# Kernel optimization log

Hardware: AMD Instinct MI355X
Metric: run time of the kernel (lower is better)

## Reference

```python
import jax, jax.numpy as jnp
import numpy as np

B, K, N, D = 64, 64, 32768, 2048   # batch, knn neighbors, memory size, feat dim (hardcoded 2048 in source)
NC, NHID, TOPK = 2048, 512, 5      # num clusters, gcn hidden, topk in affinity masking


def setup_inputs() -> dict:
    key = jax.random.key(0)
    ks = jax.random.split(key, 8)
    features = jax.random.normal(ks[0], (N, D), jnp.float32)
    labels = jax.random.randint(ks[1], (N,), 0, NC)
    indexes = jax.random.randint(ks[2], (B,), 0, N)
    ori_knn_neighbor = jax.random.randint(ks[3], (B, K), 0, N)
    s = 0.02
    conv_w = jax.random.normal(ks[4], (2 * D, NHID), jnp.float32) * s
    conv_b = jnp.zeros((NHID,), jnp.float32)
    w1 = jax.random.normal(ks[5], (NHID, NHID), jnp.float32) * s
    b1 = jnp.zeros((NHID,), jnp.float32)
    prelu_a = jnp.full((NHID,), 0.25, jnp.float32)
    w2 = jax.random.normal(ks[6], (NHID, 2), jnp.float32) * s
    b2 = jnp.zeros((2,), jnp.float32)
    return dict(indexes=indexes, features=features, labels=labels,
                ori_knn_neighbor=ori_knn_neighbor, conv_w=conv_w, conv_b=conv_b,
                w1=w1, b1=b1, prelu_a=prelu_a, w2=w2, b2=b2)


def _build_graphs(indexes, features, labels, ori_knn_neighbor):
    # cluster mean features (index_add_ + count normalize), done under no_grad in torch
    counts = jax.ops.segment_sum(jnp.ones((N,), jnp.float32), labels, num_segments=NC)
    clu_sum = jax.ops.segment_sum(features, labels, num_segments=NC)
    clu_mean = clu_sum / jnp.maximum(counts, 1.0)[:, None]

    def per_sample(idx, nbr):
        clu_lab = labels[nbr]                                  # [K]
        cf = clu_mean[clu_lab].at[0].set(features[idx])        # [K, D]
        A = (cf @ cf.T) / 5.0                                  # [K, K]
        j = jnp.arange(K)
        # keep only first occurrence of each cluster label (np.unique return_index)
        dup = jnp.any((clu_lab[:, None] == clu_lab[None, :]) & (j[None, :] < j[:, None]), axis=1)
        keep = (~dup).astype(A.dtype)                          # [K]
        _, ti = jax.lax.top_k(A, TOPK)                         # [K, TOPK]
        m = jnp.zeros_like(A).at[j[:, None], ti].set(1.0)
        m = ((m > 0) & (m.T > 0)).astype(A.dtype) * keep[:, None] * keep[None, :]
        A = A * m
        cf = cf / jnp.linalg.norm(cf, axis=1, keepdims=True)   # row-normalize
        cf = cf - cf[0]                                        # center on query (row 0 -> 0)
        return cf, A

    x, adj = jax.vmap(per_sample)(indexes, ori_knn_neighbor)   # [B,K,D], [B,K,K]
    return jax.lax.stop_gradient(x), jax.lax.stop_gradient(adj)


def reference(indexes, features, labels, ori_knn_neighbor,
              conv_w, conv_b, w1, b1, prelu_a, w2, b2):
    x, adj = _build_graphs(indexes, features, labels, ori_knn_neighbor)
    # GraphConv with MeanAggregator: agg = A @ x, concat, linear, relu
    agg = jnp.einsum('bij,bjd->bid', adj, x)                   # [B,K,D]
    h = jax.nn.relu(jnp.concatenate([x, agg], axis=-1) @ conv_w + conv_b)  # [B,K,NHID]
    h0 = h.reshape(-1, NHID)
    h1 = h0 @ w1 + b1
    h1 = jnp.where(h1 > 0, h1, prelu_a * h1)                   # PReLU(nhid)
    logits = h1 @ w2 + b2                                      # [B*K, 2]
    return jax.nn.softmax(logits.reshape(B, K, 2), axis=2)
```

## Files before the change

### kernel.cpp

```cpp
#include <hip/hip_runtime.h>
#include <hip/hip_bf16.h>

#define BB 64
#define KN 64
#define NPTS 32768
#define DD 2048
#define NCC 2048
#define NH 512
#define MM 4096
#define K2 4096

typedef unsigned short u16;
typedef unsigned int u32;
typedef __attribute__((ext_vector_type(8))) short short8;
typedef __attribute__((ext_vector_type(4))) float f32x4;

__device__ __forceinline__ float bf2f(u32 u){
  union { u32 i; float f; } v; v.i = u << 16; return v.f;
}
__device__ __forceinline__ u16 f2bf(float f){
  union { float f; u32 i; } v; v.f = f;
  u32 x = v.i;
  return (u16)((x + 0x7fffu + ((x >> 16) & 1u)) >> 16);
}

typedef __attribute__((address_space(3))) u32 as3_u32;
typedef const __attribute__((address_space(1))) u32 as1_u32;
__device__ __forceinline__ void glds16(const void* g, void* l){
  __builtin_amdgcn_global_load_lds((as1_u32*)g, (as3_u32*)l, 16, 0, 0);
}

__global__ __launch_bounds__(256) void k_prep(
    const int* __restrict__ labels, int* __restrict__ counts,
    const int* __restrict__ knn, int* __restrict__ used,
    const void* __restrict__ conv_w, u16* __restrict__ cwT, int fcw,
    const void* __restrict__ w1, u16* __restrict__ w1T, int fw1){
  __shared__ u16 tile[64][65];
  int bb = blockIdx.x, t = threadIdx.x;
  if(bb < 128){
    int n = bb*256 + t;
    atomicAdd(&counts[labels[n]], 1);
    return;
  }
  if(bb == 704){
    #pragma unroll
    for(int i=0;i<16;i++){
      int idx = i*256 + t;
      used[labels[knn[idx]]] = 1;
    }
    return;
  }
  const void* src; u16* dst; int Kd, Nd, isf32, tb;
  if(bb < 640){ src=conv_w; dst=cwT; Kd=K2; Nd=NH; isf32=fcw; tb=bb-128; }
  else        { src=w1;     dst=w1T; Kd=NH; Nd=NH; isf32=fw1; tb=bb-640; }
  int nbt = Nd >> 6;
  int k0 = (tb / nbt) << 6;
  int n0 = (tb % nbt) << 6;
  if(isf32){
    const float* s = (const float*)src;
    #pragma unroll
    for(int ph=0; ph<16; ph++){
      int idx = ph*256 + t;
      int r = idx >> 6, c = idx & 63;
      tile[r][c] = f2bf(s[(size_t)(k0+r)*Nd + n0 + c]);
    }
  } else {
    const u16* s = (const u16*)src;
    #pragma unroll
    for(int ph=0; ph<16; ph++){
      int idx = ph*256 + t;
      int r = idx >> 6, c = idx & 63;
      tile[r][c] = s[(size_t)(k0+r)*Nd + n0 + c];
    }
  }
  __syncthreads();
  #pragma unroll
  for(int ph=0; ph<16; ph++){
    int idx = ph*256 + t;
    int r = idx >> 6, c = idx & 63;
    dst[(size_t)(n0+r)*Kd + k0 + c] = tile[c][r];
  }
}

__global__ void k_scan(const int* __restrict__ counts, int* __restrict__ offsets){
  __shared__ int sb[256];
  int t = threadIdx.x;
  int c[8]; int s = 0;
  #pragma unroll
  for(int i=0;i<8;i++){ c[i] = counts[t*8+i]; s += c[i]; }
  sb[t] = s; __syncthreads();
  int v = s;
  for(int off=1; off<256; off<<=1){
    int u = (t>=off) ? sb[t-off] : 0;
    __syncthreads();
    v += u; sb[t] = v;
    __syncthreads();
  }
  int run = v - s;
  #pragma unroll
  for(int i=0;i<8;i++){ offsets[t*8+i] = run; run += c[i]; }
}

__global__ void k_scatter(const int* __restrict__ labels, const int* __restrict__ offsets,
                          int* __restrict__ cursor, int* __restrict__ sorted){
  int n = blockIdx.x*256 + threadIdx.x;
  int c = labels[n];
  int p = atomicAdd(&cursor[c], 1);
  sorted[offsets[c] + p] = n;
}

__global__ __launch_bounds__(256) void k_clumean(
    const void* __restrict__ feat, const int* __restrict__ counts,
    const int* __restrict__ offsets, const int* __restrict__ sorted,
    const int* __restrict__ used, int isf32, float* __restrict__ clu){
  int c = blockIdx.x, t = threadIdx.x;
  if(!used[c]) return;
  __shared__ int ridx[64];
  int cnt = counts[c], start = offsets[c];
  float acc[8] = {0,0,0,0,0,0,0,0};
  for(int base=0; base<cnt; base+=64){
    int take = min(64, cnt-base);
    __syncthreads();
    if(t < take) ridx[t] = sorted[start+base+t];
    __syncthreads();
    if(isf32){
      const float* ff = (const float*)feat;
      int r = 0;
      for(; r+2<=take; r+=2){
        const float* p0 = ff + (size_t)ridx[r]*DD + t*8;
        const float* p1 = ff + (size_t)ridx[r+1]*DD + t*8;
        float4 a0=*(const float4*)p0, b0=*(const float4*)(p0+4);
        float4 a1=*(const float4*)p1, b1=*(const float4*)(p1+4);
        acc[0]+=a0.x+a1.x; acc[1]+=a0.y+a1.y; acc[2]+=a0.z+a1.z; acc[3]+=a0.w+a1.w;
        acc[4]+=b0.x+b1.x; acc[5]+=b0.y+b1.y; acc[6]+=b0.z+b1.z; acc[7]+=b0.w+b1.w;
      }
      if(r < take){
        const float* p0 = ff + (size_t)ridx[r]*DD + t*8;
        float4 a0=*(const float4*)p0, b0=*(const float4*)(p0+4);
        acc[0]+=a0.x; acc[1]+=a0.y; acc[2]+=a0.z; acc[3]+=a0.w;
        acc[4]+=b0.x; acc[5]+=b0.y; acc[6]+=b0.z; acc[7]+=b0.w;
      }
    } else {
      const u16* fb = (const u16*)feat;
      int r = 0;
      for(; r+2<=take; r+=2){
        const u16* p0 = fb + (size_t)ridx[r]*DD + t*8;
        const u16* p1 = fb + (size_t)ridx[r+1]*DD + t*8;
        uint4 v0 = *(const uint4*)p0, v1 = *(const uint4*)p1;
        acc[0]+=bf2f(v0.x&0xffffu)+bf2f(v1.x&0xffffu); acc[1]+=bf2f(v0.x>>16)+bf2f(v1.x>>16);
        acc[2]+=bf2f(v0.y&0xffffu)+bf2f(v1.y&0xffffu); acc[3]+=bf2f(v0.y>>16)+bf2f(v1.y>>16);
        acc[4]+=bf2f(v0.z&0xffffu)+bf2f(v1.z&0xffffu); acc[5]+=bf2f(v0.z>>16)+bf2f(v1.z>>16);
        acc[6]+=bf2f(v0.w&0xffffu)+bf2f(v1.w&0xffffu); acc[7]+=bf2f(v0.w>>16)+bf2f(v1.w>>16);
      }
      if(r < take){
        const u16* p0 = fb + (size_t)ridx[r]*DD + t*8;
        uint4 v0 = *(const uint4*)p0;
        acc[0]+=bf2f(v0.x&0xffffu); acc[1]+=bf2f(v0.x>>16);
        acc[2]+=bf2f(v0.y&0xffffu); acc[3]+=bf2f(v0.y>>16);
        acc[4]+=bf2f(v0.z&0xffffu); acc[5]+=bf2f(v0.z>>16);
        acc[6]+=bf2f(v0.w&0xffffu); acc[7]+=bf2f(v0.w>>16);
      }
    }
  }
  float div = fmaxf((float)cnt, 1.0f);
  float* o = clu + (size_t)c*DD + t*8;
  float4 o0 = make_float4(acc[0]/div, acc[1]/div, acc[2]/div, acc[3]/div);
  float4 o1 = make_float4(acc[4]/div, acc[5]/div, acc[6]/div, acc[7]/div);
  *(float4*)o = o0;
  *(float4*)(o+4) = o1;
}

__global__ __launch_bounds__(256) void k_Apart(
    const void* __restrict__ feat, const float* __restrict__ clu,
    const int* __restrict__ indexes, const int* __restrict__ labels,
    const int* __restrict__ knn, int isf32, float* __restrict__ Apart){
  int b = blockIdx.x >> 2, g = blockIdx.x & 3;
  int t = threadIdx.x;
  __shared__ float cfT[64][68];
  __shared__ int sl[64];
  if(t < 64) sl[t] = labels[knn[b*64 + t]];
  int qidx = indexes[b];
  __syncthreads();

  int i0 = (t & 15)*4, j0 = (t >> 4)*4;
  float acc[4][4];
  #pragma unroll
  for(int a=0;a<4;a++)
    #pragma unroll
    for(int c2=0;c2<4;c2++) acc[a][c2] = 0.f;

  for(int ch=g*8; ch<g*8+8; ch++){
    int dbase = ch*64;
    #pragma unroll
    for(int ps=0; ps<16; ps++){
      int idx = ps*256 + t;
      int k = idx >> 6, dd = idx & 63;
      float v;
      if(k == 0){
        size_t fi = (size_t)qidx*DD + dbase + dd;
        v = isf32 ? ((const float*)feat)[fi] : bf2f(((const u16*)feat)[fi]);
      } else {
        v = clu[(size_t)sl[k]*DD + dbase + dd];
      }
      cfT[dd][k] = v;
    }
    __syncthreads();
    #pragma unroll 4
    for(int dd=0; dd<64; dd++){
      float4 av = *(const float4*)&cfT[dd][i0];
      float4 bv = *(const float4*)&cfT[dd][j0];
      float aa[4] = {av.x, av.y, av.z, av.w};
      float bbv[4] = {bv.x, bv.y, bv.z, bv.w};
      #pragma unroll
      for(int ii=0;ii<4;ii++)
        #pragma unroll
        for(int jj=0;jj<4;jj++)
          acc[ii][jj] += aa[ii]*bbv[jj];
    }
    __syncthreads();
  }

  float* op = Apart + ((size_t)(g*64 + b))*4096;
  #pragma unroll
  for(int ii=0;ii<4;ii++)
    *(float4*)&op[(i0+ii)*64 + j0] = make_float4(acc[ii][0], acc[ii][1], acc[ii][2], acc[ii][3]);
}

__global__ __launch_bounds__(256) void k_Afinal(
    const float* __restrict__ Apart, const int* __restrict__ labels,
    const int* __restrict__ knn,
    float* __restrict__ adj, float* __restrict__ norms){
  int b = blockIdx.x, t = threadIdx.x;
  __shared__ float A[64][65];
  __shared__ unsigned long long mb[64];
  __shared__ int sl[64];
  __shared__ int sk[64];
  if(t < 64) sl[t] = labels[knn[b*64 + t]];
  const float* P = Apart + (size_t)b*4096;
  const size_t gs = (size_t)64*4096;
  #pragma unroll
  for(int ps=0; ps<16; ps++){
    int idx = ps*256 + t;
    float s = P[idx] + P[idx+gs] + P[idx+2*gs] + P[idx+3*gs];
    A[idx>>6][idx&63] = s * 0.2f;
  }
  __syncthreads();
  if(t < 64){
    int dup = 0;
    for(int j=0;j<t;j++) dup |= (sl[j]==sl[t]);
    sk[t] = dup ? 0 : 1;
    unsigned long long chosen = 0;
    const float* row = A[t];
    #pragma unroll
    for(int p=0;p<5;p++){
      float best = -INFINITY; int bi = 0;
      for(int j=0;j<64;j++){
        bool taken = (chosen >> j) & 1ull;
        float v = row[j];
        if(!taken && v > best){ best = v; bi = j; }
      }
      chosen |= (1ull << bi);
    }
    mb[t] = chosen;
    norms[b*64+t] = sqrtf(fmaxf(A[t][t]*5.0f, 0.0f));
  }
  __syncthreads();
  float* O = adj + (size_t)b*4096;
  #pragma unroll
  for(int ps=0; ps<16; ps++){
    int idx = ps*256 + t;
    int i = idx >> 6, j = idx & 63;
    bool on = ((mb[i]>>j)&1ull) && ((mb[j]>>i)&1ull) && sk[i] && sk[j];
    O[idx] = on ? A[i][j] : 0.0f;
  }
}

__global__ __launch_bounds__(256) void k_xagg(
    const void* __restrict__ feat, const float* __restrict__ clu,
    const int* __restrict__ indexes, const int* __restrict__ labels,
    const int* __restrict__ knn, const float* __restrict__ norms,
    const float* __restrict__ adj, int isf32, u16* __restrict__ xab){
  int b = blockIdx.x >> 2, g = blockIdx.x & 3;
  int t = threadIdx.x;
  __shared__ u16  xs[64][512];
  __shared__ float adjs[64][65];
  __shared__ float nzv[64][8];
  __shared__ u16   nzj[64][8];
  __shared__ int   nzc[64];
  __shared__ int   sl[64];
  __shared__ float sn[64];

  const float* Ab = adj + (size_t)b*4096;
  #pragma unroll
  for(int ps=0; ps<16; ps++){
    int idx = ps*256 + t;
    adjs[idx>>6][idx&63] = Ab[idx];
  }
  if(t < 64){
    sl[t] = labels[knn[b*64 + t]];
    sn[t] = 1.0f / fmaxf(norms[b*64 + t], 1e-30f);
  }
  int qidx = indexes[b];
  int d = g*512 + t*2;
  float q0, q1;
  if(isf32){
    float2 qv = *(const float2*)((const float*)feat + (size_t)qidx*DD + d);
    q0 = qv.x; q1 = qv.y;
  } else {
    u32 w = *(const u32*)((const u16*)feat + (size_t)qidx*DD + d);
    q0 = bf2f(w & 0xffffu); q1 = bf2f(w >> 16);
  }
  __syncthreads();
  if(t < 64){
    int c = 0;
    for(int j=0;j<64;j++){
      float v = adjs[t][j];
      if(v != 0.0f && c < 8){ nzv[t][c] = v; nzj[t][c] = (u16)j; c++; }
    }
    nzc[t] = c;
  }
  float inv0 = sn[0];
  q0 *= inv0; q1 *= inv0;

  *(u32*)&xs[0][t*2] = 0u;
  *(u32*)(xab + (size_t)(b*64)*K2 + d) = 0u;
  for(int k=1;k<64;k++){
    float2 cv = *(const float2*)(clu + (size_t)sl[k]*DD + d);
    float invk = sn[k];
    u16 x0 = f2bf(cv.x*invk - q0), x1 = f2bf(cv.y*invk - q1);
    u32 w = (u32)x0 | ((u32)x1 << 16);
    *(u32*)&xs[k][t*2] = w;
    *(u32*)(xab + (size_t)(b*64+k)*K2 + d) = w;
  }
  __syncthreads();

  for(int r=0;r<64;r++){
    float a0 = 0.f, a1 = 0.f;
    int c = nzc[r];
    for(int p=0;p<c;p++){
      float s = nzv[r][p]; int j = nzj[r][p];
      u32 w = *(const u32*)&xs[j][t*2];
      a0 += s*bf2f(w & 0xffffu);
      a1 += s*bf2f(w >> 16);
    }
    u32 w = (u32)f2bf(a0) | ((u32)f2bf(a1) << 16);
    *(u32*)(xab + (size_t)(b*64+r)*K2 + DD + d) = w;
  }
}

template<int EPI>
__global__ __launch_bounds__(256, 2) void k_gemm(
    const u16* __restrict__ Am, const u16* __restrict__ Bt,
    const void* __restrict__ bias, const void* __restrict__ pa,
    int fbias, int fpa,
    void* __restrict__ Cout, int Md, int Nd, int Kd)
{
  __shared__ u16 As[2][64*64];
  __shared__ u16 Bs[2][64*64];
  int t = threadIdx.x;
  int nblk = gridDim.x;
  int bid = (blockIdx.x & 7)*(nblk >> 3) + (blockIdx.x >> 3);
  int nb = Nd >> 6;
  int m0 = (bid / nb) << 6;
  int n0 = (bid % nb) << 6;
  int wave = t >> 6, lane = t & 63;
  int wm = wave >> 1, wn = wave & 1;
  int lm = lane & 15, lq = lane >> 4;
  int lrow = lane >> 3, lcol = lane & 7;

  f32x4 acc[2][2];
  #pragma unroll
  for(int i=0;i<2;i++)
    #pragma unroll
    for(int j=0;j<2;j++) acc[i][j] = (f32x4){0.f,0.f,0.f,0.f};

  auto stage = [&](int buf, int kb){
    #pragma unroll
    for(int c=0;c<2;c++){
      int cb = wave*2 + c;
      int row = cb*8 + lrow;
      int col = lcol ^ (row & 7);
      glds16(Am + (size_t)(m0+row)*Kd + kb + col*8, &As[buf][cb*512]);
    }
    #pragma unroll
    for(int c=0;c<2;c++){
      int cb = wave*2 + c;
      int row = cb*8 + lrow;
      int col = lcol ^ (row & 7);
      glds16(Bt + (size_t)(n0+row)*Kd + kb + col*8, &Bs[buf][cb*512]);
    }
  };

  stage(0, 0);
  __syncthreads();
  int cur = 0;
  for(int kb=0; kb<Kd; kb+=64){
    if(kb + 64 < Kd) stage(cur^1, kb+64);
    #pragma unroll
    for(int kk=0;kk<2;kk++){
      short8 af[2], bfr[2];
      #pragma unroll
      for(int mi=0;mi<2;mi++){
        int r = wm*32 + mi*16 + lm;
        int p = ((kk<<2)+lq) ^ (r & 7);
        union{ uint4 u; short8 v; } x;
        x.u = *(const uint4*)&As[cur][r*64 + p*8];
        af[mi] = x.v;
      }
      #pragma unroll
      for(int ni=0;ni<2;ni++){
        int r = wn*32 + ni*16 + lm;
        int p = ((kk<<2)+lq) ^ (r & 7);
        union{ uint4 u; short8 v; } x;
        x.u = *(const uint4*)&Bs[cur][r*64 + p*8];
        bfr[ni] = x.v;
      }
      #pragma unroll
      for(int mi=0;mi<2;mi++)
        #pragma unroll
        for(int ni=0;ni<2;ni++)
          acc[mi][ni] = __builtin_amdgcn_mfma_f32_16x16x32_bf16(af[mi], bfr[ni], acc[mi][ni], 0, 0, 0);
    }
    __syncthreads();
    cur ^= 1;
  }

  #pragma unroll
  for(int ni=0;ni<2;ni++){
    int col = n0 + wn*32 + ni*16 + lm;
    float bs = fbias ? ((const float*)bias)[col] : bf2f(((const u16*)bias)[col]);
    float av = 0.f;
    if(EPI==1) av = fpa ? ((const float*)pa)[col] : bf2f(((const u16*)pa)[col]);
    #pragma unroll
    for(int mi=0;mi<2;mi++){
      int rowb = m0 + wm*32 + mi*16 + lq*4;
      #pragma unroll
      for(int r2=0;r2<4;r2++){
        float v = acc[mi][ni][r2] + bs;
        if(EPI==0){
          v = fmaxf(v, 0.f);
          ((u16*)Cout)[(size_t)(rowb+r2)*Nd + col] = f2bf(v);
        } else {
          v = (v > 0.f) ? v : av*v;
          ((float*)Cout)[(size_t)(rowb+r2)*Nd + col] = v;
        }
      }
    }
  }
}

__global__ __launch_bounds__(256) void k_out(
    const float* __restrict__ h1, const void* __restrict__ w2,
    const void* __restrict__ b2, int fw2, int fb2, int fo,
    void* __restrict__ out){
  int t = threadIdx.x; int lane = t & 63; int row = blockIdx.x*4 + (t >> 6);
  const float* hr = h1 + (size_t)row*NH;
  float s0 = 0.f, s1 = 0.f;
  #pragma unroll
  for(int j=0;j<NH/64;j++){
    int i = lane + j*64;
    float h = hr[i];
    float w0 = fw2 ? ((const float*)w2)[i*2+0] : bf2f(((const u16*)w2)[i*2+0]);
    float w1v= fw2 ? ((const float*)w2)[i*2+1] : bf2f(((const u16*)w2)[i*2+1]);
    s0 += h * w0;
    s1 += h * w1v;
  }
  #pragma unroll
  for(int off=32; off>0; off>>=1){
    s0 += __shfl_down(s0, off);
    s1 += __shfl_down(s1, off);
  }
  if(lane==0){
    float bb0 = fb2 ? ((const float*)b2)[0] : bf2f(((const u16*)b2)[0]);
    float bb1 = fb2 ? ((const float*)b2)[1] : bf2f(((const u16*)b2)[1]);
    float l0 = s0 + bb0;
    float l1 = s1 + bb1;
    float m = fmaxf(l0, l1);
    float e0 = expf(l0 - m), e1 = expf(l1 - m);
    float inv = 1.0f / (e0 + e1);
    if(fo){
      ((float*)out)[row*2+0] = e0*inv;
      ((float*)out)[row*2+1] = e1*inv;
    } else {
      ((u16*)out)[row*2+0] = f2bf(e0*inv);
      ((u16*)out)[row*2+1] = f2bf(e1*inv);
    }
  }
}

__global__ void k_fill_sentinel(u32* __restrict__ out, int nwords){
  int i = blockIdx.x*256 + threadIdx.x;
  if(i < nwords) out[i] = 0x40404040u;
}

extern "C" void kernel_launch(void* const* d_in, const int* in_sizes, int n_in,
                              void* d_out, int out_size, void* d_ws, size_t ws_size,
                              hipStream_t stream) {
  const int* indexes = (const int*)d_in[0];
  const void* feat   = d_in[1];
  const int* labels  = (const int*)d_in[2];
  const int* knn     = (const int*)d_in[3];
  const void* conv_w = d_in[4];
  const void* conv_b = d_in[5];
  const void* w1     = d_in[6];
  const void* b1     = d_in[7];
  const void* pa     = d_in[8];
  const void* w2     = d_in[9];
  const void* b2     = d_in[10];

  int ff  = (in_sizes[1]  != (int)((size_t)NPTS*DD*2));
  int fcw = (in_sizes[4]  != (int)((size_t)2*DD*NH*2));
  int fcb = (in_sizes[5]  != NH*2);
  int fw1 = (in_sizes[6]  != (int)((size_t)NH*NH*2));
  int fb1 = (in_sizes[7]  != NH*2);
  int fpa = (in_sizes[8]  != NH*2);
  int fw2 = (in_sizes[9]  != NH*2*2);
  int fb2 = (in_sizes[10] != 2*2);
  int fo  = (out_size     != MM*2*2);

  char* w = (char*)d_ws;
  size_t o = 0;
  auto alloc = [&](size_t bytes) -> void* {
    void* p = w + o; o = (o + bytes + 255) & ~(size_t)255; return p;
  };
  int*   counts  = (int*)  alloc((size_t)NCC*4);
  int*   cursor  = (int*)  alloc((size_t)NCC*4);
  int*   used    = (int*)  alloc((size_t)NCC*4);
  int*   offsets = (int*)  alloc((size_t)NCC*4);
  int*   sorted  = (int*)  alloc((size_t)NPTS*4);
  float* norms   = (float*)alloc((size_t)MM*4);
  float* adj     = (float*)alloc((size_t)BB*64*64*4);
  float* Apart   = (float*)alloc((size_t)4*BB*64*64*4);
  float* clu     = (float*)alloc((size_t)NCC*DD*4);
  u16*   xab     = (u16*)  alloc((size_t)MM*K2*2);
  u16*   cwT     = (u16*)  alloc((size_t)K2*NH*2);
  u16*   w1T     = (u16*)  alloc((size_t)NH*NH*2);
  u16*   hb      = (u16*)  clu;
  float* h1      = (float*)((char*)clu + (size_t)MM*NH*2);

  size_t NEED = o;
  if(ws_size < NEED){
    int nwords = out_size/4;
    k_fill_sentinel<<<(nwords+255)/256, 256, 0, stream>>>((u32*)d_out, nwords);
    return;
  }

  hipMemsetAsync(counts, 0, (size_t)NCC*4*3, stream);

  k_prep   <<<705, 256, 0, stream>>>(labels, counts, knn, used, conv_w, cwT, fcw, w1, w1T, fw1);
  k_scan   <<<1, 256, 0, stream>>>(counts, offsets);
  k_scatter<<<NPTS/256, 256, 0, stream>>>(labels, offsets, cursor, sorted);
  k_clumean<<<NCC, 256, 0, stream>>>(feat, counts, offsets, sorted, used, ff, clu);
  k_Apart  <<<BB*4, 256, 0, stream>>>(feat, clu, indexes, labels, knn, ff, Apart);
  k_Afinal <<<BB, 256, 0, stream>>>(Apart, labels, knn, adj, norms);
  k_xagg   <<<BB*4, 256, 0, stream>>>(feat, clu, indexes, labels, knn, norms, adj, ff, xab);

  k_gemm<0><<<(MM/64)*(NH/64), 256, 0, stream>>>(xab, cwT, conv_b, nullptr, fcb, 0, (void*)hb, MM, NH, K2);
  k_gemm<1><<<(MM/64)*(NH/64), 256, 0, stream>>>(hb, w1T, b1, pa, fb1, fpa, (void*)h1, MM, NH, NH);

  k_out    <<<MM/4, 256, 0, stream>>>(h1, w2, b2, fw2, fb2, fo, d_out);
}
```

Measured before the change: 558.8 us.

## Unroll cluster-mean loads, split xagg finer, and double GEMM K-tile

The fp32 cluster-mean accumulation now reads four feature rows per iteration instead of two, so more loads are in flight. The bf16 path is collapsed to a simple one-row loop. The graph feature/aggregation kernel now launches eight blocks per sample, each covering 256 columns with one element per thread, which halves its LDS tile and raises parallelism but uses narrower 16-bit global stores. The bf16 MFMA GEMM stages 128-wide K tiles instead of 64, halving barriers and loop iterations at the cost of double the LDS per block, which may lower occupancy.

Measured after the change: 533.9 us. -4.5%, faster.

```diff
diff --git a/kernel.cpp b/kernel.cpp
--- a/kernel.cpp
+++ b/kernel.cpp
@@ -126,15 +126,21 @@
     if(isf32){
       const float* ff = (const float*)feat;
       int r = 0;
-      for(; r+2<=take; r+=2){
+      for(; r+4<=take; r+=4){
         const float* p0 = ff + (size_t)ridx[r]*DD + t*8;
         const float* p1 = ff + (size_t)ridx[r+1]*DD + t*8;
+        const float* p2 = ff + (size_t)ridx[r+2]*DD + t*8;
+        const float* p3 = ff + (size_t)ridx[r+3]*DD + t*8;
         float4 a0=*(const float4*)p0, b0=*(const float4*)(p0+4);
         float4 a1=*(const float4*)p1, b1=*(const float4*)(p1+4);
-        acc[0]+=a0.x+a1.x; acc[1]+=a0.y+a1.y; acc[2]+=a0.z+a1.z; acc[3]+=a0.w+a1.w;
-        acc[4]+=b0.x+b1.x; acc[5]+=b0.y+b1.y; acc[6]+=b0.z+b1.z; acc[7]+=b0.w+b1.w;
-      }
-      if(r < take){
+        float4 a2=*(const float4*)p2, b2=*(const float4*)(p2+4);
+        float4 a3=*(const float4*)p3, b3=*(const float4*)(p3+4);
+        acc[0]+=a0.x+a1.x+a2.x+a3.x; acc[1]+=a0.y+a1.y+a2.y+a3.y;
+        acc[2]+=a0.z+a1.z+a2.z+a3.z; acc[3]+=a0.w+a1.w+a2.w+a3.w;
+        acc[4]+=b0.x+b1.x+b2.x+b3.x; acc[5]+=b0.y+b1.y+b2.y+b3.y;
+        acc[6]+=b0.z+b1.z+b2.z+b3.z; acc[7]+=b0.w+b1.w+b2.w+b3.w;
+      }
+      for(; r<take; r++){
         const float* p0 = ff + (size_t)ridx[r]*DD + t*8;
         float4 a0=*(const float4*)p0, b0=*(const float4*)(p0+4);
         acc[0]+=a0.x; acc[1]+=a0.y; acc[2]+=a0.z; acc[3]+=a0.w;
@@ -142,17 +148,7 @@
       }
     } else {
       const u16* fb = (const u16*)feat;
-      int r = 0;
-      for(; r+2<=take; r+=2){
-        const u16* p0 = fb + (size_t)ridx[r]*DD + t*8;
-        const u16* p1 = fb + (size_t)ridx[r+1]*DD + t*8;
-        uint4 v0 = *(const uint4*)p0, v1 = *(const uint4*)p1;
-        acc[0]+=bf2f(v0.x&0xffffu)+bf2f(v1.x&0xffffu); acc[1]+=bf2f(v0.x>>16)+bf2f(v1.x>>16);
-        acc[2]+=bf2f(v0.y&0xffffu)+bf2f(v1.y&0xffffu); acc[3]+=bf2f(v0.y>>16)+bf2f(v1.y>>16);
-        acc[4]+=bf2f(v0.z&0xffffu)+bf2f(v1.z&0xffffu); acc[5]+=bf2f(v0.z>>16)+bf2f(v1.z>>16);
-        acc[6]+=bf2f(v0.w&0xffffu)+bf2f(v1.w&0xffffu); acc[7]+=bf2f(v0.w>>16)+bf2f(v1.w>>16);
-      }
-      if(r < take){
+      for(int r=0; r<take; r++){
         const u16* p0 = fb + (size_t)ridx[r]*DD + t*8;
         uint4 v0 = *(const uint4*)p0;
         acc[0]+=bf2f(v0.x&0xffffu); acc[1]+=bf2f(v0.x>>16);
@@ -181,14 +177,12 @@
   if(t < 64) sl[t] = labels[knn[b*64 + t]];
   int qidx = indexes[b];
   __syncthreads();
-
   int i0 = (t & 15)*4, j0 = (t >> 4)*4;
   float acc[4][4];
   #pragma unroll
-  for(int a=0;a<4;a++)
-    #pragma unroll
-    for(int c2=0;c2<4;c2++) acc[a][c2] = 0.f;
-
+  for(int x=0;x<4;x++)
+    #pragma unroll
+    for(int c2=0;c2<4;c2++) acc[x][c2] = 0.f;
   for(int ch=g*8; ch<g*8+8; ch++){
     int dbase = ch*64;
     #pragma unroll
@@ -219,7 +213,6 @@
     }
     __syncthreads();
   }
-
   float* op = Apart + ((size_t)(g*64 + b))*4096;
   #pragma unroll
   for(int ii=0;ii<4;ii++)
@@ -280,9 +273,9 @@
     const int* __restrict__ indexes, const int* __restrict__ labels,
     const int* __restrict__ knn, const float* __restrict__ norms,
     const float* __restrict__ adj, int isf32, u16* __restrict__ xab){
-  int b = blockIdx.x >> 2, g = blockIdx.x & 3;
+  int b = blockIdx.x >> 3, g = blockIdx.x & 7;
   int t = threadIdx.x;
-  __shared__ u16  xs[64][512];
+  __shared__ u16  xs[64][256];
   __shared__ float adjs[64][65];
   __shared__ float nzv[64][8];
   __shared__ u16   nzj[64][8];
@@ -301,14 +294,12 @@
     sn[t] = 1.0f / fmaxf(norms[b*64 + t], 1e-30f);
   }
   int qidx = indexes[b];
-  int d = g*512 + t*2;
-  float q0, q1;
+  int d = g*256 + t;
+  float q0;
   if(isf32){
-    float2 qv = *(const float2*)((const float*)feat + (size_t)qidx*DD + d);
-    q0 = qv.x; q1 = qv.y;
+    q0 = ((const float*)feat)[(size_t)qidx*DD + d];
   } else {
-    u32 w = *(const u32*)((const u16*)feat + (size_t)qidx*DD + d);
-    q0 = bf2f(w & 0xffffu); q1 = bf2f(w >> 16);
+    q0 = bf2f(((const u16*)feat)[(size_t)qidx*DD + d]);
   }
   __syncthreads();
   if(t < 64){
@@ -319,32 +310,25 @@
     }
     nzc[t] = c;
   }
-  float inv0 = sn[0];
-  q0 *= inv0; q1 *= inv0;
-
-  *(u32*)&xs[0][t*2] = 0u;
-  *(u32*)(xab + (size_t)(b*64)*K2 + d) = 0u;
+  q0 *= sn[0];
+
+  xs[0][t] = 0;
+  xab[(size_t)(b*64)*K2 + d] = 0;
   for(int k=1;k<64;k++){
-    float2 cv = *(const float2*)(clu + (size_t)sl[k]*DD + d);
-    float invk = sn[k];
-    u16 x0 = f2bf(cv.x*invk - q0), x1 = f2bf(cv.y*invk - q1);
-    u32 w = (u32)x0 | ((u32)x1 << 16);
-    *(u32*)&xs[k][t*2] = w;
-    *(u32*)(xab + (size_t)(b*64+k)*K2 + d) = w;
+    float cv = clu[(size_t)sl[k]*DD + d];
+    u16 x0 = f2bf(cv*sn[k] - q0);
+    xs[k][t] = x0;
+    xab[(size_t)(b*64+k)*K2 + d] = x0;
   }
   __syncthreads();
 
   for(int r=0;r<64;r++){
-    float a0 = 0.f, a1 = 0.f;
+    float a0 = 0.f;
     int c = nzc[r];
     for(int p=0;p<c;p++){
-      float s = nzv[r][p]; int j = nzj[r][p];
-      u32 w = *(const u32*)&xs[j][t*2];
-      a0 += s*bf2f(w & 0xffffu);
-      a1 += s*bf2f(w >> 16);
-    }
-    u32 w = (u32)f2bf(a0) | ((u32)f2bf(a1) << 16);
-    *(u32*)(xab + (size_t)(b*64+r)*K2 + DD + d) = w;
+      a0 += nzv[r][p] * bf2f(xs[nzj[r][p]][t]);
+    }
+    xab[(size_t)(b*64+r)*K2 + DD + d] = f2bf(a0);
   }
 }
 
@@ -355,8 +339,8 @@
     int fbias, int fpa,
     void* __restrict__ Cout, int Md, int Nd, int Kd)
 {
-  __shared__ u16 As[2][64*64];
-  __shared__ u16 Bs[2][64*64];
+  __shared__ u16 As[2][64*128];
+  __shared__ u16 Bs[2][64*128];
   int t = threadIdx.x;
   int nblk = gridDim.x;
   int bid = (blockIdx.x & 7)*(nblk >> 3) + (blockIdx.x >> 3);
@@ -366,7 +350,7 @@
   int wave = t >> 6, lane = t & 63;
   int wm = wave >> 1, wn = wave & 1;
   int lm = lane & 15, lq = lane >> 4;
-  int lrow = lane >> 3, lcol = lane & 7;
+  int lrow4 = lane >> 4, lcol16 = lane & 15;
 
   f32x4 acc[2][2];
   #pragma unroll
@@ -376,17 +360,17 @@
 
   auto stage = [&](int buf, int kb){
     #pragma unroll
-    for(int c=0;c<2;c++){
-      int cb = wave*2 + c;
-      int row = cb*8 + lrow;
-      int col = lcol ^ (row & 7);
+    for(int c=0;c<4;c++){
+      int cb = wave*4 + c;
+      int row = cb*4 + lrow4;
+      int col = lcol16 ^ (row & 7);
       glds16(Am + (size_t)(m0+row)*Kd + kb + col*8, &As[buf][cb*512]);
     }
     #pragma unroll
-    for(int c=0;c<2;c++){
-      int cb = wave*2 + c;
-      int row = cb*8 + lrow;
-      int col = lcol ^ (row & 7);
+    for(int c=0;c<4;c++){
+      int cb = wave*4 + c;
+      int row = cb*4 + lrow4;
+      int col = lcol16 ^ (row & 7);
       glds16(Bt + (size_t)(n0+row)*Kd + kb + col*8, &Bs[buf][cb*512]);
     }
   };
@@ -394,17 +378,17 @@
   stage(0, 0);
   __syncthreads();
   int cur = 0;
-  for(int kb=0; kb<Kd; kb+=64){
-    if(kb + 64 < Kd) stage(cur^1, kb+64);
-    #pragma unroll
-    for(int kk=0;kk<2;kk++){
+  for(int kb=0; kb<Kd; kb+=128){
+    if(kb + 128 < Kd) stage(cur^1, kb+128);
+    #pragma unroll
+    for(int kk=0;kk<4;kk++){
       short8 af[2], bfr[2];
       #pragma unroll
       for(int mi=0;mi<2;mi++){
         int r = wm*32 + mi*16 + lm;
         int p = ((kk<<2)+lq) ^ (r & 7);
         union{ uint4 u; short8 v; } x;
-        x.u = *(const uint4*)&As[cur][r*64 + p*8];
+        x.u = *(const uint4*)&As[cur][r*128 + p*8];
         af[mi] = x.v;
       }
       #pragma unroll
@@ -412,7 +396,7 @@
         int r = wn*32 + ni*16 + lm;
         int p = ((kk<<2)+lq) ^ (r & 7);
         union{ uint4 u; short8 v; } x;
-        x.u = *(const uint4*)&Bs[cur][r*64 + p*8];
+        x.u = *(const uint4*)&Bs[cur][r*128 + p*8];
         bfr[ni] = x.v;
       }
       #pragma unroll
@@ -553,7 +537,7 @@
   k_clumean<<<NCC, 256, 0, stream>>>(feat, counts, offsets, sorted, used, ff, clu);
   k_Apart  <<<BB*4, 256, 0, stream>>>(feat, clu, indexes, labels, knn, ff, Apart);
   k_Afinal <<<BB, 256, 0, stream>>>(Apart, labels, knn, adj, norms);
-  k_xagg   <<<BB*4, 256, 0, stream>>>(feat, clu, indexes, labels, knn, norms, adj, ff, xab);
+  k_xagg   <<<BB*8, 256, 0, stream>>>(feat, clu, indexes, labels, knn, norms, adj, ff, xab);
 
   k_gemm<0><<<(MM/64)*(NH/64), 256, 0, stream>>>(xab, cwT, conv_b, nullptr, fcb, 0, (void*)hb, MM, NH, K2);
   k_gemm<1><<<(MM/64)*(NH/64), 256, 0, stream>>>(hb, w1T, b1, pa, fb1, fpa, (void*)h1, MM, NH, NH);
```
